# Kernel optimization log

Hardware: AMD Instinct MI355X
Metric: run time of the kernel (lower is better)

Reference implementation:

```python
import jax, jax.numpy as jnp
import numpy as np

CHANNELS = 256
NUM_HEADS = 4
NUM_GROUPS = 8
EPS = 1e-5


def setup_inputs() -> dict:
    key = jax.random.key(0)
    ks = jax.random.split(key, 7)
    c = CHANNELS
    x = jax.random.normal(ks[0], (2, c, 16, 16, 16), dtype=jnp.float32)
    # GroupNorm affine params (torch init: weight=1, bias=0)
    norm_w = jnp.ones((c,), dtype=jnp.float32)
    norm_b = jnp.zeros((c,), dtype=jnp.float32)
    # 1x1x1 Conv3d weights stored as [out_ch, in_ch]
    fan = 1.0 / np.sqrt(c)
    qkv_w = jax.random.uniform(ks[1], (3 * c, c), minval=-fan, maxval=fan, dtype=jnp.float32)
    qkv_b = jax.random.uniform(ks[2], (3 * c,), minval=-fan, maxval=fan, dtype=jnp.float32)
    proj_w = jax.random.uniform(ks[3], (c, c), minval=-fan, maxval=fan, dtype=jnp.float32)
    proj_b = jax.random.uniform(ks[4], (c,), minval=-fan, maxval=fan, dtype=jnp.float32)
    return {"x": x, "norm_w": norm_w, "norm_b": norm_b,
            "qkv_w": qkv_w, "qkv_b": qkv_b, "proj_w": proj_w, "proj_b": proj_b}


def _group_norm(x, w, b):
    B, C, D, H, W = x.shape
    g = NUM_GROUPS
    xg = x.reshape(B, g, C // g, D, H, W)
    mean = xg.mean(axis=(2, 3, 4, 5), keepdims=True)
    var = xg.var(axis=(2, 3, 4, 5), keepdims=True)
    xg = (xg - mean) * jax.lax.rsqrt(var + EPS)
    x = xg.reshape(B, C, D, H, W)
    return x * w[None, :, None, None, None] + b[None, :, None, None, None]


def _conv1x1(x, w, b):
    # x: [B, Cin, D, H, W], w: [Cout, Cin]
    y = jnp.einsum('bcdhw,oc->bodhw', x, w)
    return y + b[None, :, None, None, None]


def reference(x, norm_w, norm_b, qkv_w, qkv_b, proj_w, proj_b):
    B, C, D, H, W = x.shape
    N = D * H * W
    hd = C // NUM_HEADS
    x_norm = _group_norm(x, norm_w, norm_b)
    qkv = _conv1x1(x_norm, qkv_w, qkv_b)  # [B, 3C, D, H, W]
    q, k, v = jnp.split(qkv, 3, axis=1)
    q = q.reshape(B, NUM_HEADS, hd, N)
    k = k.reshape(B, NUM_HEADS, hd, N)
    v = v.reshape(B, NUM_HEADS, hd, N)
    scale = hd ** -0.5
    # attn[b,h,n,m] = softmax_m(q[:, :, :, n] . k[:, :, :, m] * scale)
    scores = jnp.einsum('bhcn,bhcm->bhnm', q, k) * scale
    attn = jax.nn.softmax(scores, axis=-1)
    out = jnp.einsum('bhcm,bhnm->bhcn', v, attn)
    out = out.reshape(B, C, D, H, W)
    return _conv1x1(out, proj_w, proj_b) + x
```

## Files before the change

kernel.cpp:

```cpp
#include <hip/hip_runtime.h>
#include <hip/hip_bf16.h>

#define NSP 4096
#define CH 256
#define NB 2
#define NG 8
#define CPG 32
#define NHD 4
#define HDIM 64

typedef unsigned short u16;
typedef unsigned int u32;
typedef __attribute__((ext_vector_type(8))) short bf16x8;
typedef __attribute__((ext_vector_type(4))) float f32x4;

#define MFMA __builtin_amdgcn_mfma_f32_16x16x32_bf16
#define QSCALE 0.18033688f

__device__ __forceinline__ u16 f2bf(float f) {
    u32 i = __float_as_uint(f);
    u32 r = (i + 0x7FFFu + ((i >> 16) & 1u)) >> 16;
    return (u16)r;
}

__device__ __forceinline__ void dma16(const u16* g, u16* l) {
    __builtin_amdgcn_global_load_lds(
        (const __attribute__((address_space(1))) void*)g,
        (__attribute__((address_space(3))) void*)l, 16, 0, 0);
}

__global__ __launch_bounds__(256) void prep(const float* __restrict__ qw,
                                            const float* __restrict__ pw,
                                            u16* __restrict__ wqb,
                                            u16* __restrict__ wpb,
                                            const float* __restrict__ x,
                                            float* __restrict__ partial) {
    if (blockIdx.x < 256) {
        int i = (blockIdx.x * 256 + threadIdx.x) * 4;
        const float* src; u16* dstbase; int j;
        if (i < 3 * CH * CH) { src = qw + i; dstbase = wqb; j = i; }
        else { j = i - 3 * CH * CH; src = pw + j; dstbase = wpb; }
        int m = j >> 8, c = j & 255;
        int dc = ((((c >> 3) ^ (m & 7)) << 3)) | (c & 7);
        float4 v = *(const float4*)src;
        ushort4 o;
        o.x = f2bf(v.x); o.y = f2bf(v.y); o.z = f2bf(v.z); o.w = f2bf(v.w);
        *(ushort4*)(dstbase + (m << 8) + dc) = o;
        return;
    }
    const int id = blockIdx.x - 256;
    const int bg = id >> 4, chunk = id & 15;
    const float* p = x + (size_t)bg * (CPG * NSP) + chunk * 8192;
    float s = 0.f, ss = 0.f;
    for (int i = threadIdx.x; i < 2048; i += 256) {
        float4 u = ((const float4*)p)[i];
        s += u.x + u.y + u.z + u.w;
        ss += u.x * u.x + u.y * u.y + u.z * u.z + u.w * u.w;
    }
    for (int off = 32; off > 0; off >>= 1) {
        s += __shfl_down(s, off);
        ss += __shfl_down(ss, off);
    }
    __shared__ float red[4][2];
    const int wv = threadIdx.x >> 6;
    if ((threadIdx.x & 63) == 0) { red[wv][0] = s; red[wv][1] = ss; }
    __syncthreads();
    if (threadIdx.x == 0) {
        float ts = red[0][0] + red[1][0] + red[2][0] + red[3][0];
        float tq = red[0][1] + red[1][1] + red[2][1] + red[3][1];
        partial[(bg * 16 + chunk) * 2]     = ts;
        partial[(bg * 16 + chunk) * 2 + 1] = tq;
    }
}

__global__ __launch_bounds__(256) void gn_apply_t(const float* __restrict__ x,
                                                  const float* __restrict__ partial,
                                                  const float* __restrict__ w,
                                                  const float* __restrict__ b,
                                                  u16* __restrict__ xnT) {
    __shared__ u16 T[64][72];
    const int n0 = blockIdx.x * 64, c0 = blockIdx.y * 64, bb = blockIdx.z;
    const int t = threadIdx.x;
    const int rc = t & 63;
    const int g  = t >> 6;
    const int c  = c0 + rc;
    const int bg = bb * NG + c / CPG;
    float s = 0.f, q = 0.f;
#pragma unroll
    for (int j = 0; j < 16; ++j) {
        s += partial[(bg * 16 + j) * 2];
        q += partial[(bg * 16 + j) * 2 + 1];
    }
    const float cnt = (float)(CPG * NSP);
    float mean = s / cnt;
    float var  = q / cnt - mean * mean;
    float rstd = rsqrtf(var + 1e-5f);
    float wf = w[c] * rstd, bv = b[c] - mean * wf;
    const float* px = x + ((size_t)bb * CH + c) * NSP + n0 + g * 16;
#pragma unroll
    for (int i = 0; i < 4; ++i) {
        float4 v = *(const float4*)(px + i * 4);
        T[g * 16 + i * 4 + 0][rc] = f2bf(v.x * wf + bv);
        T[g * 16 + i * 4 + 1][rc] = f2bf(v.y * wf + bv);
        T[g * 16 + i * 4 + 2][rc] = f2bf(v.z * wf + bv);
        T[g * 16 + i * 4 + 3][rc] = f2bf(v.w * wf + bv);
    }
    __syncthreads();
    int n = t >> 2, ch = (t & 3) * 16;
    uint4 o0 = *(const uint4*)&T[n][ch];
    uint4 o1 = *(const uint4*)&T[n][ch + 8];
    const int sw = n & 7;
    const int chunk0 = (c0 + ch) >> 3;
    u16* rowp = xnT + ((size_t)bb * NSP + n0 + n) * CH;
    *(uint4*)(rowp + ((chunk0 ^ sw) << 3))       = o0;
    *(uint4*)(rowp + (((chunk0 + 1) ^ sw) << 3)) = o1;
}

__global__ __launch_bounds__(256, 2) void gemm_qkv(const u16* __restrict__ Aw,
                                                   const float* __restrict__ bias,
                                                   const u16* __restrict__ xnT,
                                                   u16* __restrict__ qT,
                                                   u16* __restrict__ kT,
                                                   u16* __restrict__ v) {
    __shared__ u16 As[64][256];
    __shared__ u16 Bs[64][256];
    const int n0 = blockIdx.x * 64, m0 = blockIdx.y * 64, bb = blockIdx.z;
    const int wave = threadIdx.x >> 6, lane = threadIdx.x & 63;
    const int lq = lane & 15, quad = lane >> 4;
#pragma unroll
    for (int j = 0; j < 8; ++j) {
        int r2 = (wave * 8 + j) * 2;
        dma16(Aw + (size_t)(m0 + r2) * CH + lane * 8, &As[r2][0]);
        dma16(xnT + ((size_t)bb * NSP + n0 + r2) * CH + lane * 8, &Bs[r2][0]);
    }
    __syncthreads();
    const int wm = (wave >> 1) * 32, wn = (wave & 1) * 32;
    const int sw = lq & 7;
    f32x4 acc[2][2] = {};
#pragma unroll
    for (int kk = 0; kk < 8; ++kk) {
        bf16x8 a[2], b[2];
#pragma unroll
        for (int mt = 0; mt < 2; ++mt)
            a[mt] = *(const bf16x8*)&As[wm + mt * 16 + lq][(((kk * 4 + quad) ^ sw)) << 3];
#pragma unroll
        for (int nt = 0; nt < 2; ++nt)
            b[nt] = *(const bf16x8*)&Bs[wn + nt * 16 + lq][(((kk * 4 + quad) ^ sw)) << 3];
#pragma unroll
        for (int mt = 0; mt < 2; ++mt)
#pragma unroll
            for (int nt = 0; nt < 2; ++nt)
                acc[mt][nt] = MFMA(a[mt], b[nt], acc[mt][nt], 0, 0, 0);
    }
    const int sect = m0 >> 8;
    const int h = (m0 & 255) >> 6;
    const float osc = (sect == 0) ? QSCALE : 1.f;
#pragma unroll
    for (int im = 0; im < 2; ++im) {
        int ml = wm + im * 16 + quad * 4;
        float4 bs = *(const float4*)(bias + m0 + ml);
#pragma unroll
        for (int in = 0; in < 2; ++in) {
            int n = n0 + wn + in * 16 + lq;
            f32x4 a = acc[im][in];
            float v0 = (a[0] + bs.x) * osc, v1 = (a[1] + bs.y) * osc;
            float v2 = (a[2] + bs.z) * osc, v3 = (a[3] + bs.w) * osc;
            if (sect < 2) {
                int lc = ml >> 3, sub = ml & 7;
                int colp = ((lc ^ (n & 7)) << 3) | sub;
                u16* base = (sect ? kT : qT) +
                            (((size_t)bb * NHD + h) * NSP + n) * HDIM + colp;
                ushort4 o;
                o.x = f2bf(v0); o.y = f2bf(v1); o.z = f2bf(v2); o.w = f2bf(v3);
                *(ushort4*)base = o;
            } else {
                float vv[4] = {v0, v1, v2, v3};
#pragma unroll
                for (int r = 0; r < 4; ++r) {
                    int ch = (m0 - 512) + ml + r;
                    int pos = (n & ~63) + ((((n >> 3) & 7) ^ (ch & 7)) << 3) + (n & 7);
                    v[((size_t)bb * CH + ch) * NSP + pos] = f2bf(vv[r]);
                }
            }
        }
    }
}

__global__ __launch_bounds__(512, 2) void attn10(const u16* __restrict__ qT,
                                                 const u16* __restrict__ kT,
                                                 const u16* __restrict__ vN,
                                                 u16* __restrict__ aoT) {
    __shared__ u16 Ks[2][2][64][64];
    __shared__ u16 Vs[2][2][64][64];
    __shared__ __align__(16) char smem_ps[8 * 32 * 72 * 2];
    __shared__ float Ml[8][2][16];
    u16 (*Ps)[32][72] = reinterpret_cast<u16(*)[32][72]>(smem_ps);
    float (*Obuf)[32][68] = reinterpret_cast<float(*)[32][68]>(smem_ps);

    const int h = blockIdx.y, bb = blockIdx.z;
    const int t = threadIdx.x;
    const int wave = t >> 6, lane = t & 63;
    const int qg = wave & 3, kh = wave >> 2;
    const int lq = lane & 15, quad = lane >> 4;
    const int q_lo = blockIdx.x * 128 + qg * 32;

    const int pr = quad ^ (lq & 7);
    const u16* qrow0 = qT + (((size_t)bb * NHD + h) * NSP + q_lo + lq) * HDIM;
    bf16x8 qf[2][2];
    qf[0][0] = *(const bf16x8*)(qrow0 + pr * 8);
    qf[0][1] = *(const bf16x8*)(qrow0 + (pr ^ 4) * 8);
    qf[1][0] = *(const bf16x8*)(qrow0 + 16 * HDIM + pr * 8);
    qf[1][1] = *(const bf16x8*)(qrow0 + 16 * HDIM + (pr ^ 4) * 8);

    const u16* khead = kT + ((size_t)bb * NHD + h) * NSP * (size_t)HDIM;
    const u16* vhead = vN + ((size_t)bb * CH + h * HDIM) * NSP;

    const int sK   = (wave < 4);
    const int kh_s = (wave >> 1) & 1;
    const int rbase = (wave & 1) * 32;
    {
#pragma unroll
        for (int j = 0; j < 4; ++j) {
            int r8 = rbase + j * 8;
            if (sK) {
                dma16(khead + (size_t)(kh_s * 2048 + r8) * HDIM + lane * 8,
                      &Ks[kh_s][0][r8][0]);
            } else {
                dma16(vhead + (size_t)(r8 + (lane >> 3)) * NSP + kh_s * 2048 + (lane & 7) * 8,
                      &Vs[kh_s][0][r8][0]);
            }
        }
    }

    float l[2] = {0.f, 0.f};
    f32x4 O[2][4] = {};
    for (int kt = 0; kt < 32; ++kt) {
        const int cur = kt & 1;
        __syncthreads();
        if (kt < 31) {
            const int K1 = (kt + 1) * 64;
#pragma unroll
            for (int j = 0; j < 4; ++j) {
                int r8 = rbase + j * 8;
                if (sK) {
                    dma16(khead + (size_t)(kh_s * 2048 + K1 + r8) * HDIM + lane * 8,
                          &Ks[kh_s][cur ^ 1][r8][0]);
                } else {
                    dma16(vhead + (size_t)(r8 + (lane >> 3)) * NSP + kh_s * 2048 + K1 + (lane & 7) * 8,
                          &Vs[kh_s][cur ^ 1][r8][0]);
                }
            }
        }
        f32x4 st[2][4];
#pragma unroll
        for (int mt = 0; mt < 4; ++mt) {
            bf16x8 a0 = *(const bf16x8*)&Ks[kh][cur][mt * 16 + lq][pr * 8];
            bf16x8 a1 = *(const bf16x8*)&Ks[kh][cur][mt * 16 + lq][(pr ^ 4) * 8];
#pragma unroll
            for (int qt = 0; qt < 2; ++qt) {
                f32x4 acc = {0.f, 0.f, 0.f, 0.f};
                acc = MFMA(a0, qf[qt][0], acc, 0, 0, 0);
                acc = MFMA(a1, qf[qt][1], acc, 0, 0, 0);
                st[qt][mt] = acc;
            }
        }
#pragma unroll
        for (int qt = 0; qt < 2; ++qt) {
            float sum = 0.f;
#pragma unroll
            for (int mt = 0; mt < 4; ++mt) {
                float p0 = __builtin_amdgcn_exp2f(st[qt][mt][0]);
                float p1 = __builtin_amdgcn_exp2f(st[qt][mt][1]);
                float p2 = __builtin_amdgcn_exp2f(st[qt][mt][2]);
                float p3 = __builtin_amdgcn_exp2f(st[qt][mt][3]);
                sum += (p0 + p1) + (p2 + p3);
                u32 r0 = __float_as_uint(p0) + 0x8000u;
                u32 r1 = __float_as_uint(p1) + 0x8000u;
                u32 r2 = __float_as_uint(p2) + 0x8000u;
                u32 r3 = __float_as_uint(p3) + 0x8000u;
                uint2 pkk;
                pkk.x = __builtin_amdgcn_perm(r1, r0, 0x07060302);
                pkk.y = __builtin_amdgcn_perm(r3, r2, 0x07060302);
                *(uint2*)&Ps[wave][qt * 16 + lq][mt * 16 + quad * 4] = pkk;
            }
            l[qt] += sum;
        }
        bf16x8 pf[2][2];
        pf[0][0] = *(const bf16x8*)&Ps[wave][lq][quad * 8];
        pf[0][1] = *(const bf16x8*)&Ps[wave][lq][32 + quad * 8];
        pf[1][0] = *(const bf16x8*)&Ps[wave][16 + lq][quad * 8];
        pf[1][1] = *(const bf16x8*)&Ps[wave][16 + lq][32 + quad * 8];
#pragma unroll
        for (int mtc = 0; mtc < 4; ++mtc) {
            bf16x8 v0 = *(const bf16x8*)&Vs[kh][cur][mtc * 16 + lq][pr * 8];
            bf16x8 v1 = *(const bf16x8*)&Vs[kh][cur][mtc * 16 + lq][(pr ^ 4) * 8];
#pragma unroll
            for (int qt = 0; qt < 2; ++qt) {
                O[qt][mtc] = MFMA(v0, pf[qt][0], O[qt][mtc], 0, 0, 0);
                O[qt][mtc] = MFMA(v1, pf[qt][1], O[qt][mtc], 0, 0, 0);
            }
        }
    }
#pragma unroll
    for (int qt = 0; qt < 2; ++qt) {
        l[qt] += __shfl_xor(l[qt], 16);
        l[qt] += __shfl_xor(l[qt], 32);
    }
    if (lane < 16) { Ml[wave][0][lane] = l[0]; Ml[wave][1][lane] = l[1]; }
    __syncthreads();
    float gl[2];
    gl[0] = l[0] + Ml[wave ^ 4][0][lq];
    gl[1] = l[1] + Ml[wave ^ 4][1][lq];
    if (kh == 1) {
#pragma unroll
        for (int qt = 0; qt < 2; ++qt)
#pragma unroll
            for (int mtc = 0; mtc < 4; ++mtc)
                *(f32x4*)&Obuf[qg][qt * 16 + lq][mtc * 16 + quad * 4] = O[qt][mtc];
    }
    __syncthreads();
    if (kh == 0) {
        const int sw = lq & 7;
#pragma unroll
        for (int qt = 0; qt < 2; ++qt) {
            float linv = 1.f / gl[qt];
            u16* rowp = aoT + ((size_t)bb * NSP + q_lo + qt * 16 + lq) * CH;
#pragma unroll
            for (int mtc = 0; mtc < 4; ++mtc) {
                f32x4 sres = O[qt][mtc] +
                             *(const f32x4*)&Obuf[qg][qt * 16 + lq][mtc * 16 + quad * 4];
                ushort4 o;
                o.x = f2bf(sres[0] * linv);
                o.y = f2bf(sres[1] * linv);
                o.z = f2bf(sres[2] * linv);
                o.w = f2bf(sres[3] * linv);
                int chunk = (h << 3) | (mtc << 1) | (quad >> 1);
                int col = ((chunk ^ sw) << 3) | ((quad & 1) << 2);
                *(ushort4*)(rowp + col) = o;
            }
        }
    }
}

__global__ __launch_bounds__(256, 2) void gemm_proj(const u16* __restrict__ Aw,
                                                    const float* __restrict__ bias,
                                                    const u16* __restrict__ aoT,
                                                    const float* __restrict__ xres,
                                                    float* __restrict__ out) {
    __shared__ u16 As[64][256];
    __shared__ u16 Bs[64][256];
    const int n0 = blockIdx.x * 64, m0 = blockIdx.y * 64, bb = blockIdx.z;
    const int wave = threadIdx.x >> 6, lane = threadIdx.x & 63;
    const int lq = lane & 15, quad = lane >> 4;
#pragma unroll
    for (int j = 0; j < 8; ++j) {
        int r2 = (wave * 8 + j) * 2;
        dma16(Aw + (size_t)(m0 + r2) * CH + lane * 8, &As[r2][0]);
        dma16(aoT + ((size_t)bb * NSP + n0 + r2) * CH + lane * 8, &Bs[r2][0]);
    }
    __syncthreads();
    const int wm = (wave >> 1) * 32, wn = (wave & 1) * 32;
    const int sw = lq & 7;
    f32x4 acc[2][2] = {};
#pragma unroll
    for (int kk = 0; kk < 8; ++kk) {
        bf16x8 a[2], b[2];
#pragma unroll
        for (int mt = 0; mt < 2; ++mt)
            a[mt] = *(const bf16x8*)&As[wm + mt * 16 + lq][(((kk * 4 + quad) ^ sw)) << 3];
#pragma unroll
        for (int nt = 0; nt < 2; ++nt)
            b[nt] = *(const bf16x8*)&Bs[wn + nt * 16 + lq][(((kk * 4 + quad) ^ sw)) << 3];
#pragma unroll
        for (int mt = 0; mt < 2; ++mt)
#pragma unroll
            for (int nt = 0; nt < 2; ++nt)
                acc[mt][nt] = MFMA(a[mt], b[nt], acc[mt][nt], 0, 0, 0);
    }
#pragma unroll
    for (int im = 0; im < 2; ++im) {
        int ml = wm + im * 16 + quad * 4;
        float4 bs = *(const float4*)(bias + m0 + ml);
        float bsv[4] = {bs.x, bs.y, bs.z, bs.w};
#pragma unroll
        for (int in = 0; in < 2; ++in) {
            int n = n0 + wn + in * 16 + lq;
            f32x4 a = acc[im][in];
#pragma unroll
            for (int r = 0; r < 4; ++r) {
                size_t idx = ((size_t)bb * CH + m0 + ml + r) * NSP + n;
                out[idx] = a[r] + bsv[r] + xres[idx];
            }
        }
    }
}

extern "C" void kernel_launch(void* const* d_in, const int* in_sizes, int n_in,
                              void* d_out, int out_size, void* d_ws, size_t ws_size,
                              hipStream_t stream) {
    const float* x      = (const float*)d_in[0];
    const float* norm_w = (const float*)d_in[1];
    const float* norm_b = (const float*)d_in[2];
    const float* qkv_w  = (const float*)d_in[3];
    const float* qkv_b  = (const float*)d_in[4];
    const float* proj_w = (const float*)d_in[5];
    const float* proj_b = (const float*)d_in[6];
    float* out = (float*)d_out;

    char* w = (char*)d_ws;
    float* partial = (float*)w;
    u16* wqb = (u16*)(w + 4096);
    u16* wpb = (u16*)(w + 4096 + 393216);
    u16* xnT = (u16*)(w + 528384);
    u16* qT  = (u16*)(w + 528384 + 4194304);
    u16* kT  = (u16*)(w + 528384 + 2 * 4194304);
    u16* v   = (u16*)(w + 528384 + 3 * 4194304);
    u16* aoT = xnT;

    prep<<<dim3(512), 256, 0, stream>>>(qkv_w, proj_w, wqb, wpb, x, partial);
    gn_apply_t<<<dim3(NSP / 64, CH / 64, NB), 256, 0, stream>>>(
        x, partial, norm_w, norm_b, xnT);
    gemm_qkv<<<dim3(NSP / 64, (3 * CH) / 64, NB), 256, 0, stream>>>(
        wqb, qkv_b, xnT, qT, kT, v);
    attn10<<<dim3(NSP / 128, NHD, NB), 512, 0, stream>>>(qT, kT, v, aoT);
    gemm_proj<<<dim3(NSP / 64, CH / 64, NB), 256, 0, stream>>>(
        wpb, proj_b, aoT, x, out);
}
```

Baseline: 143.6 us.

## Merge all five stages into one cooperative persistent kernel with grid syncs

Replaces the five separate launches (prep, group-norm apply, QKV GEMM, attention, projection GEMM) with a single cooperative kernel of 256 blocks of 512 threads. The stages are separated by grid-wide barriers, and each block handles the former work items through virtual block indices, with two 256-thread halves acting as two old blocks. The aim is to remove per-launch overhead and the gaps between kernels. In exchange it uses a fixed 128KB LDS footprint that limits occupancy, and it can only use 256 blocks, so phases that had more parallelism before now run as a persistent loop.

```diff
diff --git a/kernel.cpp b/kernel.cpp
--- a/kernel.cpp
+++ b/kernel.cpp
@@ -1,5 +1,8 @@
 #include <hip/hip_runtime.h>
 #include <hip/hip_bf16.h>
+#include <hip/hip_cooperative_groups.h>
+
+namespace cg = cooperative_groups;
 
 #define NSP 4096
 #define CH 256
@@ -29,196 +32,205 @@
         (__attribute__((address_space(3))) void*)l, 16, 0, 0);
 }
 
-__global__ __launch_bounds__(256) void prep(const float* __restrict__ qw,
-                                            const float* __restrict__ pw,
-                                            u16* __restrict__ wqb,
-                                            u16* __restrict__ wpb,
-                                            const float* __restrict__ x,
-                                            float* __restrict__ partial) {
-    if (blockIdx.x < 256) {
-        int i = (blockIdx.x * 256 + threadIdx.x) * 4;
-        const float* src; u16* dstbase; int j;
-        if (i < 3 * CH * CH) { src = qw + i; dstbase = wqb; j = i; }
-        else { j = i - 3 * CH * CH; src = pw + j; dstbase = wpb; }
-        int m = j >> 8, c = j & 255;
-        int dc = ((((c >> 3) ^ (m & 7)) << 3)) | (c & 7);
-        float4 v = *(const float4*)src;
-        ushort4 o;
-        o.x = f2bf(v.x); o.y = f2bf(v.y); o.z = f2bf(v.z); o.w = f2bf(v.w);
-        *(ushort4*)(dstbase + (m << 8) + dc) = o;
-        return;
+__global__ __launch_bounds__(512, 2) void mega(
+    const float* __restrict__ qw, const float* __restrict__ pw,
+    u16* __restrict__ wqb, u16* __restrict__ wpb,
+    const float* __restrict__ x, float* __restrict__ partial,
+    const float* __restrict__ gnw, const float* __restrict__ gnb,
+    u16* __restrict__ xnT, const float* __restrict__ qkvb,
+    u16* __restrict__ qT, u16* __restrict__ kT, u16* __restrict__ vN,
+    const float* __restrict__ projb, float* __restrict__ out) {
+    cg::grid_group grid = cg::this_grid();
+    __shared__ __align__(16) char LDS[131072];
+    const int t = threadIdx.x;
+    const int blk = blockIdx.x;
+    const int half = t >> 8, t256 = t & 255;
+    const int wave = t >> 6, lane = t & 63;
+    u16* aoT = xnT;
+
+    {
+        int idx = blk * 512 + t;
+        if (idx < (4 * CH * CH) / 4) {
+            int i = idx * 4;
+            const float* src; u16* dstbase; int j;
+            if (i < 3 * CH * CH) { src = qw + i; dstbase = wqb; j = i; }
+            else { j = i - 3 * CH * CH; src = pw + j; dstbase = wpb; }
+            int m = j >> 8, c = j & 255;
+            int dc = (((c >> 3) ^ (m & 7)) << 3) | (c & 7);
+            float4 v = *(const float4*)src;
+            ushort4 o;
+            o.x = f2bf(v.x); o.y = f2bf(v.y); o.z = f2bf(v.z); o.w = f2bf(v.w);
+            *(ushort4*)(dstbase + (m << 8) + dc) = o;
+        }
+        const float* p = x + (size_t)(blk >> 4) * (CPG * NSP) + (blk & 15) * 8192;
+        float s = 0.f, ss = 0.f;
+        for (int i = t; i < 2048; i += 512) {
+            float4 u = ((const float4*)p)[i];
+            s += u.x + u.y + u.z + u.w;
+            ss += u.x * u.x + u.y * u.y + u.z * u.z + u.w * u.w;
+        }
+        for (int off = 32; off > 0; off >>= 1) {
+            s += __shfl_down(s, off);
+            ss += __shfl_down(ss, off);
+        }
+        float* red = (float*)LDS;
+        if (lane == 0) { red[wave * 2] = s; red[wave * 2 + 1] = ss; }
+        __syncthreads();
+        if (t == 0) {
+            float ts = 0.f, tq = 0.f;
+#pragma unroll
+            for (int wv = 0; wv < 8; ++wv) { ts += red[wv * 2]; tq += red[wv * 2 + 1]; }
+            partial[blk * 2] = ts; partial[blk * 2 + 1] = tq;
+        }
     }
-    const int id = blockIdx.x - 256;
-    const int bg = id >> 4, chunk = id & 15;
-    const float* p = x + (size_t)bg * (CPG * NSP) + chunk * 8192;
-    float s = 0.f, ss = 0.f;
-    for (int i = threadIdx.x; i < 2048; i += 256) {
-        float4 u = ((const float4*)p)[i];
-        s += u.x + u.y + u.z + u.w;
-        ss += u.x * u.x + u.y * u.y + u.z * u.z + u.w * u.w;
+    __threadfence();
+    grid.sync();
+
+    {
+        u16 (*T)[72] = (u16(*)[72])(LDS + half * 9216);
+        int vb = blk * 2 + half;
+        int n0 = (vb & 63) * 64;
+        int c0 = ((vb >> 6) & 3) * 64;
+        int bb = vb >> 8;
+        int rc = t256 & 63;
+        int g  = t256 >> 6;
+        int c  = c0 + rc;
+        int bg = bb * NG + c / CPG;
+        float s = 0.f, q = 0.f;
+#pragma unroll
+        for (int j = 0; j < 16; ++j) {
+            s += partial[(bg * 16 + j) * 2];
+            q += partial[(bg * 16 + j) * 2 + 1];
+        }
+        const float cnt = (float)(CPG * NSP);
+        float mean = s / cnt;
+        float var  = q / cnt - mean * mean;
+        float rstd = rsqrtf(var + 1e-5f);
+        float wf = gnw[c] * rstd, bv = gnb[c] - mean * wf;
+        const float* px = x + ((size_t)bb * CH + c) * NSP + n0 + g * 16;
+#pragma unroll
+        for (int i = 0; i < 4; ++i) {
+            float4 v = *(const float4*)(px + i * 4);
+            T[g * 16 + i * 4 + 0][rc] = f2bf(v.x * wf + bv);
+            T[g * 16 + i * 4 + 1][rc] = f2bf(v.y * wf + bv);
+            T[g * 16 + i * 4 + 2][rc] = f2bf(v.z * wf + bv);
+            T[g * 16 + i * 4 + 3][rc] = f2bf(v.w * wf + bv);
+        }
+        __syncthreads();
+        int n = t256 >> 2, ch = (t256 & 3) * 16;
+        uint4 o0 = *(const uint4*)&T[n][ch];
+        uint4 o1 = *(const uint4*)&T[n][ch + 8];
+        const int sw = n & 7;
+        const int chunk0 = (c0 + ch) >> 3;
+        u16* rowp = xnT + ((size_t)bb * NSP + n0 + n) * CH;
+        *(uint4*)(rowp + ((chunk0 ^ sw) << 3))       = o0;
+        *(uint4*)(rowp + (((chunk0 + 1) ^ sw) << 3)) = o1;
     }
-    for (int off = 32; off > 0; off >>= 1) {
-        s += __shfl_down(s, off);
-        ss += __shfl_down(ss, off);
+    __threadfence();
+    grid.sync();
+
+    {
+        u16* As = (u16*)(LDS + half * 65536);
+        u16* Bs = (u16*)(LDS + half * 65536 + 32768);
+        const int wave4 = t256 >> 6;
+        const int lq = lane & 15, quad = lane >> 4;
+        for (int it = 0; it < 3; ++it) {
+            int vb = (it * 256 + blk) * 2 + half;
+            int vbx = vb & 63, rest = vb >> 6;
+            int vby = rest % 12, bb = rest / 12;
+            int n0 = vbx * 64, m0 = vby * 64;
+            __syncthreads();
+#pragma unroll
+            for (int j = 0; j < 8; ++j) {
+                int r2 = (wave4 * 8 + j) * 2;
+                dma16(wqb + (size_t)(m0 + r2) * CH + lane * 8, As + r2 * 256);
+                dma16(xnT + ((size_t)bb * NSP + n0 + r2) * CH + lane * 8, Bs + r2 * 256);
+            }
+            __syncthreads();
+            const int wm = (wave4 >> 1) * 32, wn = (wave4 & 1) * 32;
+            const int sw = lq & 7;
+            f32x4 acc[2][2] = {};
+#pragma unroll
+            for (int kk = 0; kk < 8; ++kk) {
+                bf16x8 a[2], b[2];
+#pragma unroll
+                for (int mt = 0; mt < 2; ++mt)
+                    a[mt] = *(const bf16x8*)(As + (wm + mt * 16 + lq) * 256 +
+                                             ((((kk * 4 + quad) ^ sw)) << 3));
+#pragma unroll
+                for (int nt = 0; nt < 2; ++nt)
+                    b[nt] = *(const bf16x8*)(Bs + (wn + nt * 16 + lq) * 256 +
+                                             ((((kk * 4 + quad) ^ sw)) << 3));
+#pragma unroll
+                for (int mt = 0; mt < 2; ++mt)
+#pragma unroll
+                    for (int nt = 0; nt < 2; ++nt)
+                        acc[mt][nt] = MFMA(a[mt], b[nt], acc[mt][nt], 0, 0, 0);
+            }
+            const int sect = m0 >> 8;
+            const int h = (m0 & 255) >> 6;
+            const float osc = (sect == 0) ? QSCALE : 1.f;
+#pragma unroll
+            for (int im = 0; im < 2; ++im) {
+                int ml = wm + im * 16 + quad * 4;
+                float4 bs = *(const float4*)(qkvb + m0 + ml);
+#pragma unroll
+                for (int in = 0; in < 2; ++in) {
+                    int n = n0 + wn + in * 16 + lq;
+                    f32x4 a = acc[im][in];
+                    float v0 = (a[0] + bs.x) * osc, v1 = (a[1] + bs.y) * osc;
+                    float v2 = (a[2] + bs.z) * osc, v3 = (a[3] + bs.w) * osc;
+                    if (sect < 2) {
+                        int lc = ml >> 3, sub = ml & 7;
+                        int colp = ((lc ^ (n & 7)) << 3) | sub;
+                        u16* base = (sect ? kT : qT) +
+                                    (((size_t)bb * NHD + h) * NSP + n) * HDIM + colp;
+                        ushort4 o;
+                        o.x = f2bf(v0); o.y = f2bf(v1); o.z = f2bf(v2); o.w = f2bf(v3);
+                        *(ushort4*)base = o;
+                    } else {
+                        float vv[4] = {v0, v1, v2, v3};
+#pragma unroll
+                        for (int r = 0; r < 4; ++r) {
+                            int ch = (m0 - 512) + ml + r;
+                            int pos = (n & ~63) + ((((n >> 3) & 7) ^ (ch & 7)) << 3) + (n & 7);
+                            vN[((size_t)bb * CH + ch) * NSP + pos] = f2bf(vv[r]);
+                        }
+                    }
+                }
+            }
+        }
     }
-    __shared__ float red[4][2];
-    const int wv = threadIdx.x >> 6;
-    if ((threadIdx.x & 63) == 0) { red[wv][0] = s; red[wv][1] = ss; }
-    __syncthreads();
-    if (threadIdx.x == 0) {
-        float ts = red[0][0] + red[1][0] + red[2][0] + red[3][0];
-        float tq = red[0][1] + red[1][1] + red[2][1] + red[3][1];
-        partial[(bg * 16 + chunk) * 2]     = ts;
-        partial[(bg * 16 + chunk) * 2 + 1] = tq;
-    }
-}
-
-__global__ __launch_bounds__(256) void gn_apply_t(const float* __restrict__ x,
-                                                  const float* __restrict__ partial,
-                                                  const float* __restrict__ w,
-                                                  const float* __restrict__ b,
-                                                  u16* __restrict__ xnT) {
-    __shared__ u16 T[64][72];
-    const int n0 = blockIdx.x * 64, c0 = blockIdx.y * 64, bb = blockIdx.z;
-    const int t = threadIdx.x;
-    const int rc = t & 63;
-    const int g  = t >> 6;
-    const int c  = c0 + rc;
-    const int bg = bb * NG + c / CPG;
-    float s = 0.f, q = 0.f;
-#pragma unroll
-    for (int j = 0; j < 16; ++j) {
-        s += partial[(bg * 16 + j) * 2];
-        q += partial[(bg * 16 + j) * 2 + 1];
-    }
-    const float cnt = (float)(CPG * NSP);
-    float mean = s / cnt;
-    float var  = q / cnt - mean * mean;
-    float rstd = rsqrtf(var + 1e-5f);
-    float wf = w[c] * rstd, bv = b[c] - mean * wf;
-    const float* px = x + ((size_t)bb * CH + c) * NSP + n0 + g * 16;
-#pragma unroll
-    for (int i = 0; i < 4; ++i) {
-        float4 v = *(const float4*)(px + i * 4);
-        T[g * 16 + i * 4 + 0][rc] = f2bf(v.x * wf + bv);
-        T[g * 16 + i * 4 + 1][rc] = f2bf(v.y * wf + bv);
-        T[g * 16 + i * 4 + 2][rc] = f2bf(v.z * wf + bv);
-        T[g * 16 + i * 4 + 3][rc] = f2bf(v.w * wf + bv);
-    }
-    __syncthreads();
-    int n = t >> 2, ch = (t & 3) * 16;
-    uint4 o0 = *(const uint4*)&T[n][ch];
-    uint4 o1 = *(const uint4*)&T[n][ch + 8];
-    const int sw = n & 7;
-    const int chunk0 = (c0 + ch) >> 3;
-    u16* rowp = xnT + ((size_t)bb * NSP + n0 + n) * CH;
-    *(uint4*)(rowp + ((chunk0 ^ sw) << 3))       = o0;
-    *(uint4*)(rowp + (((chunk0 + 1) ^ sw) << 3)) = o1;
-}
-
-__global__ __launch_bounds__(256, 2) void gemm_qkv(const u16* __restrict__ Aw,
-                                                   const float* __restrict__ bias,
-                                                   const u16* __restrict__ xnT,
-                                                   u16* __restrict__ qT,
-                                                   u16* __restrict__ kT,
-                                                   u16* __restrict__ v) {
-    __shared__ u16 As[64][256];
-    __shared__ u16 Bs[64][256];
-    const int n0 = blockIdx.x * 64, m0 = blockIdx.y * 64, bb = blockIdx.z;
-    const int wave = threadIdx.x >> 6, lane = threadIdx.x & 63;
-    const int lq = lane & 15, quad = lane >> 4;
-#pragma unroll
-    for (int j = 0; j < 8; ++j) {
-        int r2 = (wave * 8 + j) * 2;
-        dma16(Aw + (size_t)(m0 + r2) * CH + lane * 8, &As[r2][0]);
-        dma16(xnT + ((size_t)bb * NSP + n0 + r2) * CH + lane * 8, &Bs[r2][0]);
-    }
-    __syncthreads();
-    const int wm = (wave >> 1) * 32, wn = (wave & 1) * 32;
-    const int sw = lq & 7;
-    f32x4 acc[2][2] = {};
-#pragma unroll
-    for (int kk = 0; kk < 8; ++kk) {
-        bf16x8 a[2], b[2];
-#pragma unroll
-        for (int mt = 0; mt < 2; ++mt)
-            a[mt] = *(const bf16x8*)&As[wm + mt * 16 + lq][(((kk * 4 + quad) ^ sw)) << 3];
-#pragma unroll
-        for (int nt = 0; nt < 2; ++nt)
-            b[nt] = *(const bf16x8*)&Bs[wn + nt * 16 + lq][(((kk * 4 + quad) ^ sw)) << 3];
-#pragma unroll
-        for (int mt = 0; mt < 2; ++mt)
-#pragma unroll
-            for (int nt = 0; nt < 2; ++nt)
-                acc[mt][nt] = MFMA(a[mt], b[nt], acc[mt][nt], 0, 0, 0);
-    }
-    const int sect = m0 >> 8;
-    const int h = (m0 & 255) >> 6;
-    const float osc = (sect == 0) ? QSCALE : 1.f;
-#pragma unroll
-    for (int im = 0; im < 2; ++im) {
-        int ml = wm + im * 16 + quad * 4;
-        float4 bs = *(const float4*)(bias + m0 + ml);
-#pragma unroll
-        for (int in = 0; in < 2; ++in) {
-            int n = n0 + wn + in * 16 + lq;
-            f32x4 a = acc[im][in];
-            float v0 = (a[0] + bs.x) * osc, v1 = (a[1] + bs.y) * osc;
-            float v2 = (a[2] + bs.z) * osc, v3 = (a[3] + bs.w) * osc;
-            if (sect < 2) {
-                int lc = ml >> 3, sub = ml & 7;
-                int colp = ((lc ^ (n & 7)) << 3) | sub;
-                u16* base = (sect ? kT : qT) +
-                            (((size_t)bb * NHD + h) * NSP + n) * HDIM + colp;
-                ushort4 o;
-                o.x = f2bf(v0); o.y = f2bf(v1); o.z = f2bf(v2); o.w = f2bf(v3);
-                *(ushort4*)base = o;
-            } else {
-                float vv[4] = {v0, v1, v2, v3};
-#pragma unroll
-                for (int r = 0; r < 4; ++r) {
-                    int ch = (m0 - 512) + ml + r;
-                    int pos = (n & ~63) + ((((n >> 3) & 7) ^ (ch & 7)) << 3) + (n & 7);
-                    v[((size_t)bb * CH + ch) * NSP + pos] = f2bf(vv[r]);
-                }
-            }
-        }
-    }
-}
-
-__global__ __launch_bounds__(512, 2) void attn10(const u16* __restrict__ qT,
-                                                 const u16* __restrict__ kT,
-                                                 const u16* __restrict__ vN,
-                                                 u16* __restrict__ aoT) {
-    __shared__ u16 Ks[2][2][64][64];
-    __shared__ u16 Vs[2][2][64][64];
-    __shared__ __align__(16) char smem_ps[8 * 32 * 72 * 2];
-    __shared__ float Ml[8][2][16];
-    u16 (*Ps)[32][72] = reinterpret_cast<u16(*)[32][72]>(smem_ps);
-    float (*Obuf)[32][68] = reinterpret_cast<float(*)[32][68]>(smem_ps);
-
-    const int h = blockIdx.y, bb = blockIdx.z;
-    const int t = threadIdx.x;
-    const int wave = t >> 6, lane = t & 63;
-    const int qg = wave & 3, kh = wave >> 2;
-    const int lq = lane & 15, quad = lane >> 4;
-    const int q_lo = blockIdx.x * 128 + qg * 32;
-
-    const int pr = quad ^ (lq & 7);
-    const u16* qrow0 = qT + (((size_t)bb * NHD + h) * NSP + q_lo + lq) * HDIM;
-    bf16x8 qf[2][2];
-    qf[0][0] = *(const bf16x8*)(qrow0 + pr * 8);
-    qf[0][1] = *(const bf16x8*)(qrow0 + (pr ^ 4) * 8);
-    qf[1][0] = *(const bf16x8*)(qrow0 + 16 * HDIM + pr * 8);
-    qf[1][1] = *(const bf16x8*)(qrow0 + 16 * HDIM + (pr ^ 4) * 8);
-
-    const u16* khead = kT + ((size_t)bb * NHD + h) * NSP * (size_t)HDIM;
-    const u16* vhead = vN + ((size_t)bb * CH + h * HDIM) * NSP;
-
-    const int sK   = (wave < 4);
-    const int kh_s = (wave >> 1) & 1;
-    const int rbase = (wave & 1) * 32;
+    __threadfence();
+    grid.sync();
+
     {
+        typedef u16 kvarr[2][64][64];
+        kvarr* Ks = (kvarr*)LDS;
+        kvarr* Vs = (kvarr*)(LDS + 32768);
+        u16 (*Ps)[32][72] = (u16(*)[32][72])(LDS + 65536);
+        float (*Obuf)[32][68] = (float(*)[32][68])(LDS + 65536);
+        float (*Ml)[2][16] = (float(*)[2][16])(LDS + 102400);
+
+        const int qx = blk & 31, h = (blk >> 5) & 3, bb = blk >> 7;
+        const int qg = wave & 3, kh = wave >> 2;
+        const int lq = lane & 15, quad = lane >> 4;
+        const int q_lo = qx * 128 + qg * 32;
+
+        const int pr = quad ^ (lq & 7);
+        const u16* qrow0 = qT + (((size_t)bb * NHD + h) * NSP + q_lo + lq) * HDIM;
+        bf16x8 qf[2][2];
+        qf[0][0] = *(const bf16x8*)(qrow0 + pr * 8);
+        qf[0][1] = *(const bf16x8*)(qrow0 + (pr ^ 4) * 8);
+        qf[1][0] = *(const bf16x8*)(qrow0 + 16 * HDIM + pr * 8);
+        qf[1][1] = *(const bf16x8*)(qrow0 + 16 * HDIM + (pr ^ 4) * 8);
+
+        const u16* khead = kT + ((size_t)bb * NHD + h) * NSP * (size_t)HDIM;
+        const u16* vhead = vN + ((size_t)bb * CH + h * HDIM) * NSP;
+
+        const int sK   = (wave < 4);
+        const int kh_s = (wave >> 1) & 1;
+        const int rbase = (wave & 1) * 32;
 #pragma unroll
         for (int j = 0; j < 4; ++j) {
             int r8 = rbase + j * 8;
@@ -230,166 +242,168 @@
                       &Vs[kh_s][0][r8][0]);
             }
         }
+
+        float l[2] = {0.f, 0.f};
+        f32x4 O[2][4] = {};
+        for (int kt = 0; kt < 32; ++kt) {
+            const int cur = kt & 1;
+            __syncthreads();
+            if (kt < 31) {
+                const int K1 = (kt + 1) * 64;
+#pragma unroll
+                for (int j = 0; j < 4; ++j) {
+                    int r8 = rbase + j * 8;
+                    if (sK) {
+                        dma16(khead + (size_t)(kh_s * 2048 + K1 + r8) * HDIM + lane * 8,
+                              &Ks[kh_s][cur ^ 1][r8][0]);
+                    } else {
+                        dma16(vhead + (size_t)(r8 + (lane >> 3)) * NSP + kh_s * 2048 + K1 + (lane & 7) * 8,
+                              &Vs[kh_s][cur ^ 1][r8][0]);
+                    }
+                }
+            }
+            f32x4 st[2][4];
+#pragma unroll
+            for (int mt = 0; mt < 4; ++mt) {
+                bf16x8 a0 = *(const bf16x8*)&Ks[kh][cur][mt * 16 + lq][pr * 8];
+                bf16x8 a1 = *(const bf16x8*)&Ks[kh][cur][mt * 16 + lq][(pr ^ 4) * 8];
+#pragma unroll
+                for (int qt = 0; qt < 2; ++qt) {
+                    f32x4 acc = {0.f, 0.f, 0.f, 0.f};
+                    acc = MFMA(a0, qf[qt][0], acc, 0, 0, 0);
+                    acc = MFMA(a1, qf[qt][1], acc, 0, 0, 0);
+                    st[qt][mt] = acc;
+                }
+            }
+#pragma unroll
+            for (int qt = 0; qt < 2; ++qt) {
+                float sum = 0.f;
+#pragma unroll
+                for (int mt = 0; mt < 4; ++mt) {
+                    float p0 = __builtin_amdgcn_exp2f(st[qt][mt][0]);
+                    float p1 = __builtin_amdgcn_exp2f(st[qt][mt][1]);
+                    float p2 = __builtin_amdgcn_exp2f(st[qt][mt][2]);
+                    float p3 = __builtin_amdgcn_exp2f(st[qt][mt][3]);
+                    sum += (p0 + p1) + (p2 + p3);
+                    u32 r0 = __float_as_uint(p0) + 0x8000u;
+                    u32 r1 = __float_as_uint(p1) + 0x8000u;
+                    u32 r2 = __float_as_uint(p2) + 0x8000u;
+                    u32 r3 = __float_as_uint(p3) + 0x8000u;
+                    uint2 pkk;
+                    pkk.x = __builtin_amdgcn_perm(r1, r0, 0x07060302);
+                    pkk.y = __builtin_amdgcn_perm(r3, r2, 0x07060302);
+                    *(uint2*)&Ps[wave][qt * 16 + lq][mt * 16 + quad * 4] = pkk;
+                }
+                l[qt] += sum;
+            }
+            bf16x8 pf[2][2];
+            pf[0][0] = *(const bf16x8*)&Ps[wave][lq][quad * 8];
+            pf[0][1] = *(const bf16x8*)&Ps[wave][lq][32 + quad * 8];
+            pf[1][0] = *(const bf16x8*)&Ps[wave][16 + lq][quad * 8];
+            pf[1][1] = *(const bf16x8*)&Ps[wave][16 + lq][32 + quad * 8];
+#pragma unroll
+            for (int mtc = 0; mtc < 4; ++mtc) {
+                bf16x8 v0 = *(const bf16x8*)&Vs[kh][cur][mtc * 16 + lq][pr * 8];
+                bf16x8 v1 = *(const bf16x8*)&Vs[kh][cur][mtc * 16 + lq][(pr ^ 4) * 8];
+#pragma unroll
+                for (int qt = 0; qt < 2; ++qt) {
+                    O[qt][mtc] = MFMA(v0, pf[qt][0], O[qt][mtc], 0, 0, 0);
+                    O[qt][mtc] = MFMA(v1, pf[qt][1], O[qt][mtc], 0, 0, 0);
+                }
+            }
+        }
+#pragma unroll
+        for (int qt = 0; qt < 2; ++qt) {
+            l[qt] += __shfl_xor(l[qt], 16);
+            l[qt] += __shfl_xor(l[qt], 32);
+        }
+        if (lane < 16) { Ml[wave][0][lane] = l[0]; Ml[wave][1][lane] = l[1]; }
+        __syncthreads();
+        float gl[2];
+        gl[0] = l[0] + Ml[wave ^ 4][0][lq];
+        gl[1] = l[1] + Ml[wave ^ 4][1][lq];
+        if (kh == 1) {
+#pragma unroll
+            for (int qt = 0; qt < 2; ++qt)
+#pragma unroll
+                for (int mtc = 0; mtc < 4; ++mtc)
+                    *(f32x4*)&Obuf[qg][qt * 16 + lq][mtc * 16 + quad * 4] = O[qt][mtc];
+        }
+        __syncthreads();
+        if (kh == 0) {
+            const int sw = lq & 7;
+#pragma unroll
+            for (int qt = 0; qt < 2; ++qt) {
+                float linv = 1.f / gl[qt];
+                u16* rowp = aoT + ((size_t)bb * NSP + q_lo + qt * 16 + lq) * CH;
+#pragma unroll
+                for (int mtc = 0; mtc < 4; ++mtc) {
+                    f32x4 sres = O[qt][mtc] +
+                                 *(const f32x4*)&Obuf[qg][qt * 16 + lq][mtc * 16 + quad * 4];
+                    ushort4 o;
+                    o.x = f2bf(sres[0] * linv);
+                    o.y = f2bf(sres[1] * linv);
+                    o.z = f2bf(sres[2] * linv);
+                    o.w = f2bf(sres[3] * linv);
+                    int chunk = (h << 3) | (mtc << 1) | (quad >> 1);
+                    int col = ((chunk ^ sw) << 3) | ((quad & 1) << 2);
+                    *(ushort4*)(rowp + col) = o;
+                }
+            }
+        }
     }
-
-    float l[2] = {0.f, 0.f};
-    f32x4 O[2][4] = {};
-    for (int kt = 0; kt < 32; ++kt) {
-        const int cur = kt & 1;
+    __threadfence();
+    grid.sync();
+
+    {
+        u16* As = (u16*)(LDS + half * 65536);
+        u16* Bs = (u16*)(LDS + half * 65536 + 32768);
+        const int wave4 = t256 >> 6;
+        const int lq = lane & 15, quad = lane >> 4;
+        int vb = blk * 2 + half;
+        int vbx = vb & 63, vby = (vb >> 6) & 3, bb = vb >> 8;
+        int n0 = vbx * 64, m0 = vby * 64;
+#pragma unroll
+        for (int j = 0; j < 8; ++j) {
+            int r2 = (wave4 * 8 + j) * 2;
+            dma16(wpb + (size_t)(m0 + r2) * CH + lane * 8, As + r2 * 256);
+            dma16(aoT + ((size_t)bb * NSP + n0 + r2) * CH + lane * 8, Bs + r2 * 256);
+        }
         __syncthreads();
-        if (kt < 31) {
-            const int K1 = (kt + 1) * 64;
-#pragma unroll
-            for (int j = 0; j < 4; ++j) {
-                int r8 = rbase + j * 8;
-                if (sK) {
-                    dma16(khead + (size_t)(kh_s * 2048 + K1 + r8) * HDIM + lane * 8,
-                          &Ks[kh_s][cur ^ 1][r8][0]);
-                } else {
-                    dma16(vhead + (size_t)(r8 + (lane >> 3)) * NSP + kh_s * 2048 + K1 + (lane & 7) * 8,
-                          &Vs[kh_s][cur ^ 1][r8][0]);
-                }
-            }
-        }
-        f32x4 st[2][4];
-#pragma unroll
-        for (int mt = 0; mt < 4; ++mt) {
-            bf16x8 a0 = *(const bf16x8*)&Ks[kh][cur][mt * 16 + lq][pr * 8];
-            bf16x8 a1 = *(const bf16x8*)&Ks[kh][cur][mt * 16 + lq][(pr ^ 4) * 8];
-#pragma unroll
-            for (int qt = 0; qt < 2; ++qt) {
-                f32x4 acc = {0.f, 0.f, 0.f, 0.f};
-                acc = MFMA(a0, qf[qt][0], acc, 0, 0, 0);
-                acc = MFMA(a1, qf[qt][1], acc, 0, 0, 0);
-                st[qt][mt] = acc;
-            }
-        }
-#pragma unroll
-        for (int qt = 0; qt < 2; ++qt) {
-            float sum = 0.f;
-#pragma unroll
-            for (int mt = 0; mt < 4; ++mt) {
-                float p0 = __builtin_amdgcn_exp2f(st[qt][mt][0]);
-                float p1 = __builtin_amdgcn_exp2f(st[qt][mt][1]);
-                float p2 = __builtin_amdgcn_exp2f(st[qt][mt][2]);
-                float p3 = __builtin_amdgcn_exp2f(st[qt][mt][3]);
-                sum += (p0 + p1) + (p2 + p3);
-                u32 r0 = __float_as_uint(p0) + 0x8000u;
-                u32 r1 = __float_as_uint(p1) + 0x8000u;
-                u32 r2 = __float_as_uint(p2) + 0x8000u;
-                u32 r3 = __float_as_uint(p3) + 0x8000u;
-                uint2 pkk;
-                pkk.x = __builtin_amdgcn_perm(r1, r0, 0x07060302);
-                pkk.y = __builtin_amdgcn_perm(r3, r2, 0x07060302);
-                *(uint2*)&Ps[wave][qt * 16 + lq][mt * 16 + quad * 4] = pkk;
-            }
-            l[qt] += sum;
-        }
-        bf16x8 pf[2][2];
-        pf[0][0] = *(const bf16x8*)&Ps[wave][lq][quad * 8];
-        pf[0][1] = *(const bf16x8*)&Ps[wave][lq][32 + quad * 8];
-        pf[1][0] = *(const bf16x8*)&Ps[wave][16 + lq][quad * 8];
-        pf[1][1] = *(const bf16x8*)&Ps[wave][16 + lq][32 + quad * 8];
-#pragma unroll
-        for (int mtc = 0; mtc < 4; ++mtc) {
-            bf16x8 v0 = *(const bf16x8*)&Vs[kh][cur][mtc * 16 + lq][pr * 8];
-            bf16x8 v1 = *(const bf16x8*)&Vs[kh][cur][mtc * 16 + lq][(pr ^ 4) * 8];
-#pragma unroll
-            for (int qt = 0; qt < 2; ++qt) {
-                O[qt][mtc] = MFMA(v0, pf[qt][0], O[qt][mtc], 0, 0, 0);
-                O[qt][mtc] = MFMA(v1, pf[qt][1], O[qt][mtc], 0, 0, 0);
-            }
-        }
-    }
-#pragma unroll
-    for (int qt = 0; qt < 2; ++qt) {
-        l[qt] += __shfl_xor(l[qt], 16);
-        l[qt] += __shfl_xor(l[qt], 32);
-    }
-    if (lane < 16) { Ml[wave][0][lane] = l[0]; Ml[wave][1][lane] = l[1]; }
-    __syncthreads();
-    float gl[2];
-    gl[0] = l[0] + Ml[wave ^ 4][0][lq];
-    gl[1] = l[1] + Ml[wave ^ 4][1][lq];
-    if (kh == 1) {
-#pragma unroll
-        for (int qt = 0; qt < 2; ++qt)
-#pragma unroll
-            for (int mtc = 0; mtc < 4; ++mtc)
-                *(f32x4*)&Obuf[qg][qt * 16 + lq][mtc * 16 + quad * 4] = O[qt][mtc];
-    }
-    __syncthreads();
-    if (kh == 0) {
+        const int wm = (wave4 >> 1) * 32, wn = (wave4 & 1) * 32;
         const int sw = lq & 7;
-#pragma unroll
-        for (int qt = 0; qt < 2; ++qt) {
-            float linv = 1.f / gl[qt];
-            u16* rowp = aoT + ((size_t)bb * NSP + q_lo + qt * 16 + lq) * CH;
-#pragma unroll
-            for (int mtc = 0; mtc < 4; ++mtc) {
-                f32x4 sres = O[qt][mtc] +
-                             *(const f32x4*)&Obuf[qg][qt * 16 + lq][mtc * 16 + quad * 4];
-                ushort4 o;
-                o.x = f2bf(sres[0] * linv);
-                o.y = f2bf(sres[1] * linv);
-                o.z = f2bf(sres[2] * linv);
-                o.w = f2bf(sres[3] * linv);
-                int chunk = (h << 3) | (mtc << 1) | (quad >> 1);
-                int col = ((chunk ^ sw) << 3) | ((quad & 1) << 2);
-                *(ushort4*)(rowp + col) = o;
-            }
-        }
-    }
-}
-
-__global__ __launch_bounds__(256, 2) void gemm_proj(const u16* __restrict__ Aw,
-                                                    const float* __restrict__ bias,
-                                                    const u16* __restrict__ aoT,
-                                                    const float* __restrict__ xres,
-                                                    float* __restrict__ out) {
-    __shared__ u16 As[64][256];
-    __shared__ u16 Bs[64][256];
-    const int n0 = blockIdx.x * 64, m0 = blockIdx.y * 64, bb = blockIdx.z;
-    const int wave = threadIdx.x >> 6, lane = threadIdx.x & 63;
-    const int lq = lane & 15, quad = lane >> 4;
-#pragma unroll
-    for (int j = 0; j < 8; ++j) {
-        int r2 = (wave * 8 + j) * 2;
-        dma16(Aw + (size_t)(m0 + r2) * CH + lane * 8, &As[r2][0]);
-        dma16(aoT + ((size_t)bb * NSP + n0 + r2) * CH + lane * 8, &Bs[r2][0]);
-    }
-    __syncthreads();
-    const int wm = (wave >> 1) * 32, wn = (wave & 1) * 32;
-    const int sw = lq & 7;
-    f32x4 acc[2][2] = {};
-#pragma unroll
-    for (int kk = 0; kk < 8; ++kk) {
-        bf16x8 a[2], b[2];
-#pragma unroll
-        for (int mt = 0; mt < 2; ++mt)
-            a[mt] = *(const bf16x8*)&As[wm + mt * 16 + lq][(((kk * 4 + quad) ^ sw)) << 3];
-#pragma unroll
-        for (int nt = 0; nt < 2; ++nt)
-            b[nt] = *(const bf16x8*)&Bs[wn + nt * 16 + lq][(((kk * 4 + quad) ^ sw)) << 3];
-#pragma unroll
-        for (int mt = 0; mt < 2; ++mt)
+        f32x4 acc[2][2] = {};
+#pragma unroll
+        for (int kk = 0; kk < 8; ++kk) {
+            bf16x8 a[2], b[2];
+#pragma unroll
+            for (int mt = 0; mt < 2; ++mt)
+                a[mt] = *(const bf16x8*)(As + (wm + mt * 16 + lq) * 256 +
+                                         ((((kk * 4 + quad) ^ sw)) << 3));
 #pragma unroll
             for (int nt = 0; nt < 2; ++nt)
-                acc[mt][nt] = MFMA(a[mt], b[nt], acc[mt][nt], 0, 0, 0);
-    }
-#pragma unroll
-    for (int im = 0; im < 2; ++im) {
-        int ml = wm + im * 16 + quad * 4;
-        float4 bs = *(const float4*)(bias + m0 + ml);
-        float bsv[4] = {bs.x, bs.y, bs.z, bs.w};
-#pragma unroll
-        for (int in = 0; in < 2; ++in) {
-            int n = n0 + wn + in * 16 + lq;
-            f32x4 a = acc[im][in];
-#pragma unroll
-            for (int r = 0; r < 4; ++r) {
-                size_t idx = ((size_t)bb * CH + m0 + ml + r) * NSP + n;
-                out[idx] = a[r] + bsv[r] + xres[idx];
+                b[nt] = *(const bf16x8*)(Bs + (wn + nt * 16 + lq) * 256 +
+                                         ((((kk * 4 + quad) ^ sw)) << 3));
+#pragma unroll
+            for (int mt = 0; mt < 2; ++mt)
+#pragma unroll
+                for (int nt = 0; nt < 2; ++nt)
+                    acc[mt][nt] = MFMA(a[mt], b[nt], acc[mt][nt], 0, 0, 0);
+        }
+#pragma unroll
+        for (int im = 0; im < 2; ++im) {
+            int ml = wm + im * 16 + quad * 4;
+            float4 bs = *(const float4*)(projb + m0 + ml);
+            float bsv[4] = {bs.x, bs.y, bs.z, bs.w};
+#pragma unroll
+            for (int in = 0; in < 2; ++in) {
+                int n = n0 + wn + in * 16 + lq;
+                f32x4 a = acc[im][in];
+#pragma unroll
+                for (int r = 0; r < 4; ++r) {
+                    size_t idx = ((size_t)bb * CH + m0 + ml + r) * NSP + n;
+                    out[idx] = a[r] + bsv[r] + x[idx];
+                }
             }
         }
     }
@@ -415,14 +429,14 @@
     u16* qT  = (u16*)(w + 528384 + 4194304);
     u16* kT  = (u16*)(w + 528384 + 2 * 4194304);
     u16* v   = (u16*)(w + 528384 + 3 * 4194304);
-    u16* aoT = xnT;
-
-    prep<<<dim3(512), 256, 0, stream>>>(qkv_w, proj_w, wqb, wpb, x, partial);
-    gn_apply_t<<<dim3(NSP / 64, CH / 64, NB), 256, 0, stream>>>(
-        x, partial, norm_w, norm_b, xnT);
-    gemm_qkv<<<dim3(NSP / 64, (3 * CH) / 64, NB), 256, 0, stream>>>(
-        wqb, qkv_b, xnT, qT, kT, v);
-    attn10<<<dim3(NSP / 128, NHD, NB), 512, 0, stream>>>(qT, kT, v, aoT);
-    gemm_proj<<<dim3(NSP / 64, CH / 64, NB), 256, 0, stream>>>(
-        wpb, proj_b, aoT, x, out);
+    u16* aoT = xnT; (void)aoT;
+
+    void* args[] = {
+        (void*)&qkv_w, (void*)&proj_w, (void*)&wqb, (void*)&wpb,
+        (void*)&x, (void*)&partial, (void*)&norm_w, (void*)&norm_b,
+        (void*)&xnT, (void*)&qkv_b, (void*)&qT, (void*)&kT, (void*)&v,
+        (void*)&proj_b, (void*)&out
+    };
+    hipLaunchCooperativeKernel((const void*)mega, dim3(256), dim3(512),
+                               args, 0, stream);
 }
```

New measurement: 436.9 us. 204% more time.
